# Performance work log

Measured on AMD Instinct MI355X. Metric: run time of the kernel, lower is better.

## Reference

```python
import jax, jax.numpy as jnp
import numpy as np

N_SPIKES = 16384
N_UNITS = 256
N_NEIGHB = 128
RANK = 5
NC = 64
NC_OBS = 12
N_CAND = 10  # n_candidates*(n_search+1)+n_explore = 3*3+1
D = RANK * NC_OBS
LOG2PI = 1.8378770664093453


def setup_inputs() -> dict:
    key = jax.random.key(0)
    ks = jax.random.split(key, 8)
    features = jax.random.normal(ks[0], (N_SPIKES, RANK, NC_OBS), dtype=jnp.float32)
    mu = jax.random.normal(ks[1], (N_UNITS, RANK, NC), dtype=jnp.float32)
    # PSD inverse marginal covariances per neighborhood: A A^T / D + I
    A = jax.random.normal(ks[2], (N_NEIGHB, D, D), dtype=jnp.float32)
    Coo_inv = jnp.einsum('nij,nkj->nik', A, A) / D + jnp.eye(D, dtype=jnp.float32)
    # logdet of Coo = -logdet(Coo_inv)
    sign, ld = jnp.linalg.slogdet(Coo_inv)
    Coo_logdet = (-ld).astype(jnp.float32)
    log_proportions = jax.nn.log_softmax(jax.random.normal(ks[3], (N_UNITS,), dtype=jnp.float32))
    noise_log_prop = jnp.float32(-3.0)
    cands = jax.random.randint(ks[4], (N_SPIKES, N_CAND), 0, N_UNITS)
    nid = jax.random.randint(ks[5], (N_SPIKES,), 0, N_NEIGHB)
    # distinct observed channels per neighborhood, sorted
    perm = jnp.argsort(jax.random.uniform(ks[6], (N_NEIGHB, NC)), axis=1)
    obs_ix = jnp.sort(perm[:, :NC_OBS], axis=1)
    return {
        'features': features, 'mu': mu, 'Coo_inv': Coo_inv,
        'Coo_logdet': Coo_logdet, 'log_proportions': log_proportions,
        'noise_log_prop': noise_log_prop, 'cands': cands, 'nid': nid,
        'obs_ix': obs_ix,
    }


def reference(features, mu, Coo_inv, Coo_logdet, log_proportions, noise_log_prop, cands, nid, obs_ix):
    N, R, nco = features.shape
    Nu = mu.shape[0]
    C = cands.shape[1]
    Dd = R * nco
    # --- gather per-spike / per-candidate tables (load_batch) ---
    obs = obs_ix[nid]                                   # (N, nco)
    mu_c = mu[cands]                                    # (N, C, R, NC)
    nu = jnp.take_along_axis(mu_c, obs[:, None, None, :], axis=3)  # (N, C, R, nco)
    Cinv = Coo_inv[nid]                                 # (N, D, D)
    base = Coo_logdet[nid] + Dd * LOG2PI                # (N,)
    # --- truncated Gaussian log-likelihoods (te_batch) ---
    xf = features.reshape(N, Dd)
    xc = xf[:, None, :] - nu.reshape(N, C, Dd)          # (N, C, D)
    y = jnp.einsum('nde,nce->ncd', Cinv, xc)
    mahal = jnp.einsum('ncd,ncd->nc', y, xc)
    ll = log_proportions[cands] - 0.5 * (base[:, None] + mahal)
    yn = jnp.einsum('nde,ne->nd', Cinv, xf)
    mahal_noise = jnp.einsum('nd,nd->n', yn, xf)
    ll_noise = noise_log_prop - 0.5 * (base + mahal_noise)
    logliks = jnp.concatenate([ll, ll_noise[:, None]], axis=1)  # (N, C+1)
    Q = jax.nn.softmax(logliks, axis=1)
    # --- scatter-add sufficient statistics per unit ---
    Qc = Q[:, :C]
    seg = cands.reshape(-1)
    counts = jax.ops.segment_sum(Qc.reshape(-1), seg, num_segments=Nu)
    xw = (Qc[:, :, None] * xf[:, None, :]).reshape(N * C, Dd)
    xsum = jax.ops.segment_sum(xw, seg, num_segments=Nu)
    return jnp.concatenate([counts[:, None], xsum], axis=1)  # (Nu, D+1)
```

## Files before the change

kernel.cpp:

```cpp
#include <hip/hip_runtime.h>

#define N_SPIKES 16384
#define N_UNITS  256
#define N_NEIGHB 128
#define RANK     5
#define NC       64
#define NC_OBS   12
#define N_CAND   10
#define DD       60
#define DD4      15
#define OUT_COLS 61
#define OUT_SIZE (N_UNITS * OUT_COLS)
#define CAP      1024
#define CNT_PAD  16

__global__ __launch_bounds__(512) void precompute_kernel(
    const float* __restrict__ mu, const float* __restrict__ Coo_inv,
    const int* __restrict__ obs_ix, const float* __restrict__ log_prop,
    float* __restrict__ w_buf, float* __restrict__ b_buf)
{
    __shared__ float nu_lds[128 * 61];
    __shared__ float q2_lds[128 * 4];

    const int b   = blockIdx.x;
    const int h   = b >> 1;
    const int ub  = (b & 1) * 128;
    const int tid = threadIdx.x;

    {
        const int ut  = tid >> 2;
        const int dqt = tid & 3;
        const float* __restrict__ mub = mu + (ub + ut) * (RANK * NC);
#pragma unroll
        for (int j = 0; j < DD4; ++j) {
            const int d = dqt * DD4 + j;
            const int r = d / NC_OBS;
            const int jj = d - r * NC_OBS;
            const int ch = obs_ix[h * NC_OBS + jj];
            nu_lds[ut * 61 + d] = mub[r * NC + ch];
        }
    }
    __syncthreads();

    const int lane  = tid & 63;
    const int wave  = tid >> 6;
    const int ug    = wave >> 2;
    const int dq    = __builtin_amdgcn_readfirstlane(wave & 3);
    const int u_loc = ug * 64 + lane;
    const int u     = ub + u_loc;
    const int p     = h * N_UNITS + u;

    const float* __restrict__ Crow_base = Coo_inv + h * DD * DD + dq * DD4;

    float wreg[DD4];
#pragma unroll
    for (int j = 0; j < DD4; ++j) wreg[j] = 0.f;

    for (int e = 0; e < DD; ++e) {
        const float nu_e = nu_lds[u_loc * 61 + e];
        const float* __restrict__ Crow = Crow_base + e * DD;
#pragma unroll
        for (int j = 0; j < DD4; ++j)
            wreg[j] = fmaf(Crow[j], nu_e, wreg[j]);
    }

    float q2 = 0.f;
#pragma unroll
    for (int j = 0; j < DD4; ++j) q2 += wreg[j] * nu_lds[u_loc * 61 + dq * DD4 + j];
    q2_lds[u_loc * 4 + dq] = q2;

    float* __restrict__ wp = w_buf + p * DD + dq * DD4;
#pragma unroll
    for (int j = 0; j < DD4; ++j) wp[j] = wreg[j];

    __syncthreads();
    if ((wave & 3) == 0) {
        const float q2s = q2_lds[u_loc * 4 + 0] + q2_lds[u_loc * 4 + 1]
                        + q2_lds[u_loc * 4 + 2] + q2_lds[u_loc * 4 + 3];
        b_buf[p] = log_prop[u] - 0.5f * q2s;
    }
}

__global__ __launch_bounds__(1024) void spike_bin_kernel(
    const float* __restrict__ features, const float* __restrict__ noise_lp,
    const int* __restrict__ cands, const int* __restrict__ nid,
    const float* __restrict__ w_buf, const float* __restrict__ b_buf,
    int* __restrict__ gcount, int2* __restrict__ bins)
{
    const int tid  = threadIdx.x;
    const int lane = tid & 63;
    const int wave = tid >> 6;
    const int c    = lane & 15;
    const int s    = lane >> 4;
    const int n    = blockIdx.x * 64 + wave * 4 + s;
    const bool act = (c < N_CAND);
    const int cc   = act ? c : (N_CAND - 1);

    const float4* __restrict__ f4 = (const float4*)features;
    const float4* __restrict__ w4 = (const float4*)w_buf;

    const int   h   = nid[n];
    const float nlp = noise_lp[0];
    const int   uc  = cands[n * N_CAND + cc];
    const int   p   = h * N_UNITS + uc;
    const float bb  = b_buf[p];

    float t = 0.f;
#pragma unroll
    for (int k = 0; k < DD4; ++k) {
        const float4 wv = w4[p * DD4 + k];
        const float4 xv = f4[n * DD4 + k];
        t += wv.x * xv.x + wv.y * xv.y + wv.z * xv.z + wv.w * xv.w;
    }
    float ll = act ? (bb + t) : -3.4e38f;

    float m = ll;
    m = fmaxf(m, __shfl_xor(m, 1, 16));
    m = fmaxf(m, __shfl_xor(m, 2, 16));
    m = fmaxf(m, __shfl_xor(m, 4, 16));
    m = fmaxf(m, __shfl_xor(m, 8, 16));
    m = fmaxf(m, nlp);
    const float e = act ? __expf(ll - m) : 0.f;
    float ssum = e;
    ssum += __shfl_xor(ssum, 1, 16);
    ssum += __shfl_xor(ssum, 2, 16);
    ssum += __shfl_xor(ssum, 4, 16);
    ssum += __shfl_xor(ssum, 8, 16);
    ssum += __expf(nlp - m);
    const float q = e / ssum;

    if (act && q > 0.f) {
        const int pos = atomicAdd(&gcount[uc * CNT_PAD], 1);
        if (pos < CAP) bins[uc * CAP + pos] = make_int2(n, __float_as_int(q));
    }
}

__global__ __launch_bounds__(512) void unit_accum_kernel(
    const float* __restrict__ features, const int* __restrict__ gcount,
    const int2* __restrict__ bins, float* __restrict__ out)
{
    __shared__ int2  rec[CAP];
    __shared__ float red[8][OUT_COLS];

    const int u   = blockIdx.x;
    const int tid = threadIdx.x;
    int cnt = gcount[u * CNT_PAD];
    cnt = cnt < CAP ? cnt : CAP;

    for (int i = tid; i < cnt; i += 512) rec[i] = bins[u * CAP + i];
    __syncthreads();

    const int lane = tid & 63;
    const int wave = tid >> 6;
    const int g    = tid >> 4;
    const int l    = lane & 15;

    const float4* __restrict__ f4 = (const float4*)features;
    float4 a = {0.f, 0.f, 0.f, 0.f};
    float sq = 0.f;

#pragma unroll 2
    for (int i = g; i < cnt; i += 32) {
        const int2 r = rec[i];
        const float q = __int_as_float(r.y);
        if (l < DD4) {
            const float4 xv = f4[r.x * DD4 + l];
            a.x = fmaf(q, xv.x, a.x);
            a.y = fmaf(q, xv.y, a.y);
            a.z = fmaf(q, xv.z, a.z);
            a.w = fmaf(q, xv.w, a.w);
        } else if (l == DD4) {
            sq += q;
        }
    }

    a.x += __shfl_xor(a.x, 16, 64);  a.x += __shfl_xor(a.x, 32, 64);
    a.y += __shfl_xor(a.y, 16, 64);  a.y += __shfl_xor(a.y, 32, 64);
    a.z += __shfl_xor(a.z, 16, 64);  a.z += __shfl_xor(a.z, 32, 64);
    a.w += __shfl_xor(a.w, 16, 64);  a.w += __shfl_xor(a.w, 32, 64);
    sq  += __shfl_xor(sq, 16, 64);   sq  += __shfl_xor(sq, 32, 64);

    if (lane < DD4) {
        red[wave][1 + 4*lane + 0] = a.x;
        red[wave][1 + 4*lane + 1] = a.y;
        red[wave][1 + 4*lane + 2] = a.z;
        red[wave][1 + 4*lane + 3] = a.w;
    } else if (lane == DD4) {
        red[wave][0] = sq;
    }
    __syncthreads();

    if (tid < OUT_COLS) {
        float ssum = 0.f;
#pragma unroll
        for (int w = 0; w < 8; ++w) ssum += red[w][tid];
        out[u * OUT_COLS + tid] = ssum;
    }
}

extern "C" void kernel_launch(void* const* d_in, const int* in_sizes, int n_in,
                              void* d_out, int out_size, void* d_ws, size_t ws_size,
                              hipStream_t stream) {
    const float* features    = (const float*)d_in[0];
    const float* mu          = (const float*)d_in[1];
    const float* Coo_inv     = (const float*)d_in[2];
    const float* log_prop    = (const float*)d_in[4];
    const float* noise_lp    = (const float*)d_in[5];
    const int*   cands       = (const int*)d_in[6];
    const int*   nid         = (const int*)d_in[7];
    const int*   obs_ix      = (const int*)d_in[8];
    float* out = (float*)d_out;

    char* ws = (char*)d_ws;
    float* w_buf  = (float*)ws;
    float* b_buf  = (float*)(ws + 7864320);
    int*   gcount = (int*)(ws + 7995392);
    int2*  bins   = (int2*)(ws + 8011776);

    hipMemsetAsync(gcount, 0, N_UNITS * CNT_PAD * sizeof(int), stream);
    precompute_kernel<<<256, 512, 0, stream>>>(mu, Coo_inv, obs_ix, log_prop,
                                               w_buf, b_buf);
    spike_bin_kernel<<<256, 1024, 0, stream>>>(features, noise_lp, cands, nid,
                                               w_buf, b_buf, gcount, bins);
    unit_accum_kernel<<<256, 512, 0, stream>>>(features, gcount, bins, out);
}
```

Baseline: 116.9 us.

## Shard per-unit atomic bin counters into sub-bins and fold memset into precompute

Splits each unit's global atomic counter and bin into 8 sub-bins chosen by block index. The aim is to reduce contention on the hot atomics in the spike binning kernel. The accumulation kernel now gathers the sub-bins into shared memory using prefix offsets. The counter zeroing moves from a separate memset into the precompute kernel, which saves one launch. Each sub-bin is capped at 192 entries, so a skewed load could overflow a sub-bin and drop records where the old single cap of 1024 would not.

```diff
diff --git a/kernel.cpp b/kernel.cpp
--- a/kernel.cpp
+++ b/kernel.cpp
@@ -11,13 +11,16 @@
 #define DD4      15
 #define OUT_COLS 61
 #define OUT_SIZE (N_UNITS * OUT_COLS)
+#define NSB      8
+#define SCAP     192
+#define CNT_PAD  4
 #define CAP      1024
-#define CNT_PAD  16
 
 __global__ __launch_bounds__(512) void precompute_kernel(
     const float* __restrict__ mu, const float* __restrict__ Coo_inv,
     const int* __restrict__ obs_ix, const float* __restrict__ log_prop,
-    float* __restrict__ w_buf, float* __restrict__ b_buf)
+    float* __restrict__ w_buf, float* __restrict__ b_buf,
+    int* __restrict__ gcount)
 {
     __shared__ float nu_lds[128 * 61];
     __shared__ float q2_lds[128 * 4];
@@ -26,6 +29,8 @@
     const int h   = b >> 1;
     const int ub  = (b & 1) * 128;
     const int tid = threadIdx.x;
+
+    if (tid < 32) gcount[b * 32 + tid] = 0;
 
     {
         const int ut  = tid >> 2;
@@ -93,6 +98,7 @@
     const int c    = lane & 15;
     const int s    = lane >> 4;
     const int n    = blockIdx.x * 64 + wave * 4 + s;
+    const int sb   = blockIdx.x & (NSB - 1);
     const bool act = (c < N_CAND);
     const int cc   = act ? c : (N_CAND - 1);
 
@@ -130,8 +136,9 @@
     const float q = e / ssum;
 
     if (act && q > 0.f) {
-        const int pos = atomicAdd(&gcount[uc * CNT_PAD], 1);
-        if (pos < CAP) bins[uc * CAP + pos] = make_int2(n, __float_as_int(q));
+        const int bi  = uc * NSB + sb;
+        const int pos = atomicAdd(&gcount[bi * CNT_PAD], 1);
+        if (pos < SCAP) bins[bi * SCAP + pos] = make_int2(n, __float_as_int(q));
     }
 }
 
@@ -141,26 +148,45 @@
 {
     __shared__ int2  rec[CAP];
     __shared__ float red[8][OUT_COLS];
-
-    const int u   = blockIdx.x;
-    const int tid = threadIdx.x;
-    int cnt = gcount[u * CNT_PAD];
-    cnt = cnt < CAP ? cnt : CAP;
-
-    for (int i = tid; i < cnt; i += 512) rec[i] = bins[u * CAP + i];
-    __syncthreads();
-
+    __shared__ int   cnts[NSB];
+    __shared__ int   offs[NSB + 1];
+
+    const int u    = blockIdx.x;
+    const int tid  = threadIdx.x;
     const int lane = tid & 63;
     const int wave = tid >> 6;
-    const int g    = tid >> 4;
-    const int l    = lane & 15;
+
+    if (tid < NSB) {
+        int c = gcount[(u * NSB + tid) * CNT_PAD];
+        cnts[tid] = c < SCAP ? c : SCAP;
+    }
+    __syncthreads();
+    if (tid == 0) {
+        int o = 0;
+#pragma unroll
+        for (int sb = 0; sb < NSB; ++sb) { offs[sb] = o; o += cnts[sb]; }
+        offs[NSB] = o;
+    }
+    __syncthreads();
+
+    {
+        const int base = offs[wave];
+        const int cnt  = cnts[wave];
+        const int2* __restrict__ src = bins + (u * NSB + wave) * SCAP;
+        for (int i = lane; i < cnt; i += 64) rec[base + i] = src[i];
+    }
+    __syncthreads();
+
+    const int total = offs[NSB];
+    const int g = tid >> 4;
+    const int l = lane & 15;
 
     const float4* __restrict__ f4 = (const float4*)features;
     float4 a = {0.f, 0.f, 0.f, 0.f};
     float sq = 0.f;
 
 #pragma unroll 2
-    for (int i = g; i < cnt; i += 32) {
+    for (int i = g; i < total; i += 32) {
         const int2 r = rec[i];
         const float q = __int_as_float(r.y);
         if (l < DD4) {
@@ -215,11 +241,10 @@
     float* w_buf  = (float*)ws;
     float* b_buf  = (float*)(ws + 7864320);
     int*   gcount = (int*)(ws + 7995392);
-    int2*  bins   = (int2*)(ws + 8011776);
-
-    hipMemsetAsync(gcount, 0, N_UNITS * CNT_PAD * sizeof(int), stream);
+    int2*  bins   = (int2*)(ws + 8028160);
+
     precompute_kernel<<<256, 512, 0, stream>>>(mu, Coo_inv, obs_ix, log_prop,
-                                               w_buf, b_buf);
+                                               w_buf, b_buf, gcount);
     spike_bin_kernel<<<256, 1024, 0, stream>>>(features, noise_lp, cands, nid,
                                                w_buf, b_buf, gcount, bins);
     unit_accum_kernel<<<256, 512, 0, stream>>>(features, gcount, bins, out);
```

After: 112.4 us. 1.04x faster.
